# Optimization experiments

Measured on AMD Instinct MI355X. Metric: run time of the kernel, lower is better.

The kernel has to match this reference:

```python
import jax, jax.numpy as jnp
import numpy as np

B, K, T = 8, 88, 32768
NMS_KSIZE = 3
GAUSS_KSIZE = 7
GAUSS_STD = 1.0
VEL_PAD_L = 1
VEL_PAD_R = 1


def setup_inputs() -> dict:
    key = jax.random.key(0)
    k1, k2 = jax.random.split(key)
    onset_probs = jax.random.uniform(k1, (B, K, T), dtype=jnp.float32)
    velmap = jax.random.uniform(k2, (B, K, T), dtype=jnp.float32)
    pthresh = jnp.float32(0.5)
    return {"onset_probs": onset_probs, "velmap": velmap, "pthresh": pthresh}


def _gauss_blur1d(x, ksize, std):
    # depthwise gaussian blur along t, reflect padding, 'same' output
    center = (ksize - 1) / 2.0
    i = jnp.arange(ksize, dtype=jnp.float32)
    w = jnp.exp(-0.5 * ((i - center) / std) ** 2)
    w = w / w.sum()
    h = ksize // 2
    xp = jnp.pad(x, ((0, 0), (0, 0), (h, h)), mode="reflect")
    t = x.shape[-1]
    out = w[0] * jax.lax.dynamic_slice_in_dim(xp, 0, t, axis=2)
    for d in range(1, ksize):
        out = out + w[d] * jax.lax.dynamic_slice_in_dim(xp, d, t, axis=2)
    return out


def _nms1d(x, ksize, pthresh):
    # keep entries equal to the local max over a window of ksize (stride 1),
    # zero everything else, then threshold
    h = ksize // 2
    neg_inf = jnp.array(-jnp.inf, dtype=x.dtype)
    xp = jnp.pad(x, ((0, 0), (0, 0), (h, h)), constant_values=neg_inf)
    t = x.shape[-1]
    pooled = jax.lax.dynamic_slice_in_dim(xp, 0, t, axis=2)
    for d in range(1, ksize):
        pooled = jnp.maximum(pooled, jax.lax.dynamic_slice_in_dim(xp, d, t, axis=2))
    out = jnp.where(x == pooled, x, jnp.zeros((), x.dtype))
    out = jnp.where(out >= pthresh, out, jnp.zeros((), x.dtype))
    return out


def _windowed_vel(velmap, pad_l, pad_r):
    # mean of velmap over [t-pad_l, t+pad_r] with reflect padding (dense form
    # of read_velocities evaluated at every (b,k,t))
    total = pad_l + pad_r + 1
    vp = jnp.pad(velmap, ((0, 0), (0, 0), (pad_l, pad_r)), mode="reflect")
    t = velmap.shape[-1]
    acc = jax.lax.dynamic_slice_in_dim(vp, 0, t, axis=2)
    for d in range(1, total):
        acc = acc + jax.lax.dynamic_slice_in_dim(vp, d, t, axis=2)
    return acc / total


def reference(onset_probs, velmap, pthresh):
    prev_max = onset_probs.max()
    blurred = _gauss_blur1d(onset_probs, GAUSS_KSIZE, GAUSS_STD)
    probs = jnp.where(prev_max > 0, blurred, onset_probs)
    probs = _nms1d(probs, NMS_KSIZE, pthresh)
    vels = _windowed_vel(velmap, VEL_PAD_L, VEL_PAD_R)
    vels = jnp.where(probs > 0, vels, jnp.zeros((), vels.dtype))
    # dense equivalent of the nonzero()+gather+DataFrame: (prob, vel) at every
    # detected onset (nonzero entries of probs), zeros elsewhere
    return probs, vels
```

## Files before the change

### kernel.cpp

```cpp
#include <hip/hip_runtime.h>
#include <math.h>
#include <stdint.h>

#define T_DIM 32768
#define TILE 1024
#define BLOCK 256


__device__ __forceinline__ uint32_t float_key(float f) {
    uint32_t u = __float_as_uint(f);
    return (u & 0x80000000u) ? ~u : (u | 0x80000000u);
}


__global__ void init_ws_kernel(uint32_t* ws) { ws[0] = 0u; }

__global__ void max_kernel(const float* __restrict__ x, uint32_t* __restrict__ ws, int n4) {
    int idx = blockIdx.x * blockDim.x + threadIdx.x;
    int stride = gridDim.x * blockDim.x;
    float m = -INFINITY;
    const float4* x4 = reinterpret_cast<const float4*>(x);
    for (int i = idx; i < n4; i += stride) {
        float4 v = x4[i];
        m = fmaxf(m, fmaxf(fmaxf(v.x, v.y), fmaxf(v.z, v.w)));
    }
    #pragma unroll
    for (int off = 32; off > 0; off >>= 1)
        m = fmaxf(m, __shfl_xor(m, off));
    if ((threadIdx.x & 63) == 0)
        atomicMax(ws, float_key(m));
}

__global__ __launch_bounds__(BLOCK) void fused_kernel(
    const float* __restrict__ onset, const float* __restrict__ vel,
    const float* __restrict__ pth, const uint32_t* __restrict__ ws,
    float* __restrict__ probs_out, float* __restrict__ vels_out,
    float w0, float w1, float w2, float w3, float w4, float w5, float w6) {

    __shared__ float sx[TILE + 8];
    __shared__ float sv[TILE + 2];
    __shared__ float sp[TILE + 2];

    const int row = blockIdx.y;
    const int t0 = blockIdx.x * TILE;
    const size_t base = (size_t)row * T_DIM;
    const int tid = threadIdx.x;

    for (int i = tid; i < TILE + 8; i += BLOCK) {
        int t = t0 + i - 4;
        if (t < 0) t = -t;
        if (t >= T_DIM) t = 2 * T_DIM - 2 - t;
        sx[i] = onset[base + t];
    }
    for (int i = tid; i < TILE + 2; i += BLOCK) {
        int t = t0 + i - 1;
        if (t < 0) t = -t;
        if (t >= T_DIM) t = 2 * T_DIM - 2 - t;
        sv[i] = vel[base + t];
    }
    __syncthreads();

    const bool sel = (ws[0] > 0x80000000u);

    for (int i = tid; i < TILE + 2; i += BLOCK) {
        int t = t0 + i - 1;
        float p;
        if (t < 0 || t >= T_DIM) {
            p = -INFINITY;
        } else {
            float acc = __fmul_rn(w0, sx[i]);
            acc = __fadd_rn(acc, __fmul_rn(w1, sx[i + 1]));
            acc = __fadd_rn(acc, __fmul_rn(w2, sx[i + 2]));
            acc = __fadd_rn(acc, __fmul_rn(w3, sx[i + 3]));
            acc = __fadd_rn(acc, __fmul_rn(w4, sx[i + 4]));
            acc = __fadd_rn(acc, __fmul_rn(w5, sx[i + 5]));
            acc = __fadd_rn(acc, __fmul_rn(w6, sx[i + 6]));
            p = sel ? acc : sx[i + 3];
        }
        sp[i] = p;
    }
    __syncthreads();

    const float pthresh = pth[0];
    float po[4], vo[4];
    const int j0 = tid * 4;
    #pragma unroll
    for (int j = 0; j < 4; ++j) {
        const int i = j0 + j + 1;
        float p = sp[i];
        float pooled = fmaxf(fmaxf(sp[i - 1], p), sp[i + 1]);
        float o = (p == pooled) ? p : 0.0f;
        o = (o >= pthresh) ? o : 0.0f;
        po[j] = o;
        float a = __fadd_rn(__fadd_rn(sv[j0 + j], sv[j0 + j + 1]), sv[j0 + j + 2]);
        float v = __fdiv_rn(a, 3.0f);
        vo[j] = (o > 0.0f) ? v : 0.0f;
    }
    *reinterpret_cast<float4*>(&probs_out[base + t0 + j0]) =
        make_float4(po[0], po[1], po[2], po[3]);
    *reinterpret_cast<float4*>(&vels_out[base + t0 + j0]) =
        make_float4(vo[0], vo[1], vo[2], vo[3]);
}


extern "C" void kernel_launch(void* const* d_in, const int* in_sizes, int n_in,
                              void* d_out, int out_size, void* d_ws, size_t ws_size,
                              hipStream_t stream) {
    const float* onset = (const float*)d_in[0];
    const float* vel   = (const float*)d_in[1];
    const float* pth   = (const float*)d_in[2];

    const int n = in_sizes[0];
    const int rows = n / T_DIM;
    float* probs_out = (float*)d_out;
    float* vels_out  = probs_out + (size_t)n;
    uint32_t* wsu = (uint32_t*)d_ws;

    float e[7];
    for (int i = 0; i < 7; ++i) {
        float xi = (float)i - 3.0f;
        float arg = -0.5f * (xi * xi);
        e[i] = (float)exp((double)arg);
    }
    float s = e[0];
    for (int i = 1; i < 7; ++i) s += e[i];
    float w[7];
    for (int i = 0; i < 7; ++i) w[i] = e[i] / s;

    init_ws_kernel<<<1, 1, 0, stream>>>(wsu);
    max_kernel<<<1024, BLOCK, 0, stream>>>(onset, wsu, n / 4);

    dim3 grid(T_DIM / TILE, rows);
    fused_kernel<<<grid, BLOCK, 0, stream>>>(
        onset, vel, pth, wsu, probs_out, vels_out,
        w[0], w[1], w[2], w[3], w[4], w[5], w[6]);
}
```

Measured before the change: 398.3 us.

## Replace shared-memory tiling with per-thread vector loads and nontemporal stores

The fused kernel drops its shared-memory staging and both barriers. Each thread now loads three overlapping float4 vectors of onset and velocity from global memory and computes the blur, NMS and velocity mean in registers. Outputs are written with nontemporal stores, and the max kernel reduces within the block before doing one atomic per block. The overlapping loads triple L1/L2 read traffic per element in exchange for removing LDS traffic and synchronisation, and asm barriers keep the blur's floating-point order exact.

```diff
diff --git a/kernel.cpp b/kernel.cpp
--- a/kernel.cpp
+++ b/kernel.cpp
@@ -2,9 +2,14 @@
 #include <math.h>
 #include <stdint.h>
 
+#pragma clang fp contract(off)
+
 #define T_DIM 32768
-#define TILE 1024
 #define BLOCK 256
+
+typedef float v4f __attribute__((ext_vector_type(4)));
+
+#define FP_BARRIER(x) asm("" : "+v"(x))
 
 
 __device__ __forceinline__ uint32_t float_key(float f) {
@@ -12,23 +17,50 @@
     return (u & 0x80000000u) ? ~u : (u | 0x80000000u);
 }
 
+__device__ __forceinline__ int reflect_idx(int t) {
+    if (t < 0) t = -t;
+    if (t >= T_DIM) t = 2 * T_DIM - 2 - t;
+    return t;
+}
+
+__device__ __forceinline__ float blur7(const float* __restrict__ w,
+                                       const float* taps) {
+    float acc = w[0] * taps[0];
+    FP_BARRIER(acc);
+    #pragma unroll
+    for (int d = 1; d < 7; ++d) {
+        float p = w[d] * taps[d];
+        FP_BARRIER(p);
+        acc = acc + p;
+        FP_BARRIER(acc);
+    }
+    return acc;
+}
+
 
 __global__ void init_ws_kernel(uint32_t* ws) { ws[0] = 0u; }
 
-__global__ void max_kernel(const float* __restrict__ x, uint32_t* __restrict__ ws, int n4) {
+__global__ __launch_bounds__(BLOCK) void max_kernel(const float* __restrict__ x,
+                                                    uint32_t* __restrict__ ws, int n4) {
     int idx = blockIdx.x * blockDim.x + threadIdx.x;
     int stride = gridDim.x * blockDim.x;
     float m = -INFINITY;
-    const float4* x4 = reinterpret_cast<const float4*>(x);
+    const v4f* x4 = reinterpret_cast<const v4f*>(x);
     for (int i = idx; i < n4; i += stride) {
-        float4 v = x4[i];
+        v4f v = x4[i];
         m = fmaxf(m, fmaxf(fmaxf(v.x, v.y), fmaxf(v.z, v.w)));
     }
     #pragma unroll
     for (int off = 32; off > 0; off >>= 1)
         m = fmaxf(m, __shfl_xor(m, off));
-    if ((threadIdx.x & 63) == 0)
+    __shared__ float red[BLOCK / 64];
+    if ((threadIdx.x & 63) == 0) red[threadIdx.x >> 6] = m;
+    __syncthreads();
+    if (threadIdx.x == 0) {
+        #pragma unroll
+        for (int w = 1; w < BLOCK / 64; ++w) m = fmaxf(m, red[w]);
         atomicMax(ws, float_key(m));
+    }
 }
 
 __global__ __launch_bounds__(BLOCK) void fused_kernel(
@@ -37,69 +69,67 @@
     float* __restrict__ probs_out, float* __restrict__ vels_out,
     float w0, float w1, float w2, float w3, float w4, float w5, float w6) {
 
-    __shared__ float sx[TILE + 8];
-    __shared__ float sv[TILE + 2];
-    __shared__ float sp[TILE + 2];
-
     const int row = blockIdx.y;
-    const int t0 = blockIdx.x * TILE;
+    const int j0 = (blockIdx.x * BLOCK + threadIdx.x) * 4;
     const size_t base = (size_t)row * T_DIM;
-    const int tid = threadIdx.x;
-
-    for (int i = tid; i < TILE + 8; i += BLOCK) {
-        int t = t0 + i - 4;
-        if (t < 0) t = -t;
-        if (t >= T_DIM) t = 2 * T_DIM - 2 - t;
-        sx[i] = onset[base + t];
-    }
-    for (int i = tid; i < TILE + 2; i += BLOCK) {
-        int t = t0 + i - 1;
-        if (t < 0) t = -t;
-        if (t >= T_DIM) t = 2 * T_DIM - 2 - t;
-        sv[i] = vel[base + t];
-    }
-    __syncthreads();
 
     const bool sel = (ws[0] > 0x80000000u);
+    const float pthresh = pth[0];
+    const float w[7] = {w0, w1, w2, w3, w4, w5, w6};
 
-    for (int i = tid; i < TILE + 2; i += BLOCK) {
-        int t = t0 + i - 1;
-        float p;
-        if (t < 0 || t >= T_DIM) {
-            p = -INFINITY;
-        } else {
-            float acc = __fmul_rn(w0, sx[i]);
-            acc = __fadd_rn(acc, __fmul_rn(w1, sx[i + 1]));
-            acc = __fadd_rn(acc, __fmul_rn(w2, sx[i + 2]));
-            acc = __fadd_rn(acc, __fmul_rn(w3, sx[i + 3]));
-            acc = __fadd_rn(acc, __fmul_rn(w4, sx[i + 4]));
-            acc = __fadd_rn(acc, __fmul_rn(w5, sx[i + 5]));
-            acc = __fadd_rn(acc, __fmul_rn(w6, sx[i + 6]));
-            p = sel ? acc : sx[i + 3];
+    float pb[6], vv[6];
+
+    if (j0 >= 4 && j0 + 8 <= T_DIM) {
+        const v4f* x4 = reinterpret_cast<const v4f*>(onset + base + j0 - 4);
+        v4f A = x4[0], Bv = x4[1], C = x4[2];
+        float xx[12] = {A.x, A.y, A.z, A.w, Bv.x, Bv.y, Bv.z, Bv.w, C.x, C.y, C.z, C.w};
+
+        const v4f* v4 = reinterpret_cast<const v4f*>(vel + base + j0 - 4);
+        v4f Vm = v4[0], Vc = v4[1], Vp = v4[2];
+        vv[0] = Vm.w; vv[1] = Vc.x; vv[2] = Vc.y; vv[3] = Vc.z; vv[4] = Vc.w; vv[5] = Vp.x;
+
+        #pragma unroll
+        for (int q = 0; q < 6; ++q) {
+            float acc = blur7(w, &xx[q]);
+            pb[q] = sel ? acc : xx[q + 3];
         }
-        sp[i] = p;
+    } else {
+        const float* x = onset + base;
+        const float* v = vel + base;
+        #pragma unroll
+        for (int q = 0; q < 6; ++q) {
+            int t = j0 + q - 1;
+            vv[q] = v[reflect_idx(t)];
+            if (t < 0 || t >= T_DIM) {
+                pb[q] = -INFINITY;
+            } else {
+                float taps[7];
+                #pragma unroll
+                for (int d = 0; d < 7; ++d)
+                    taps[d] = x[reflect_idx(t - 3 + d)];
+                float acc = blur7(w, taps);
+                pb[q] = sel ? acc : x[t];
+            }
+        }
     }
-    __syncthreads();
 
-    const float pthresh = pth[0];
     float po[4], vo[4];
-    const int j0 = tid * 4;
     #pragma unroll
     for (int j = 0; j < 4; ++j) {
-        const int i = j0 + j + 1;
-        float p = sp[i];
-        float pooled = fmaxf(fmaxf(sp[i - 1], p), sp[i + 1]);
+        float p = pb[j + 1];
+        float pooled = fmaxf(fmaxf(pb[j], pb[j + 1]), pb[j + 2]);
         float o = (p == pooled) ? p : 0.0f;
         o = (o >= pthresh) ? o : 0.0f;
         po[j] = o;
-        float a = __fadd_rn(__fadd_rn(sv[j0 + j], sv[j0 + j + 1]), sv[j0 + j + 2]);
-        float v = __fdiv_rn(a, 3.0f);
-        vo[j] = (o > 0.0f) ? v : 0.0f;
+        float a = (vv[j] + vv[j + 1]) + vv[j + 2];
+        float vmean = a / 3.0f;
+        vo[j] = (o > 0.0f) ? vmean : 0.0f;
     }
-    *reinterpret_cast<float4*>(&probs_out[base + t0 + j0]) =
-        make_float4(po[0], po[1], po[2], po[3]);
-    *reinterpret_cast<float4*>(&vels_out[base + t0 + j0]) =
-        make_float4(vo[0], vo[1], vo[2], vo[3]);
+
+    v4f pov = {po[0], po[1], po[2], po[3]};
+    v4f vov = {vo[0], vo[1], vo[2], vo[3]};
+    __builtin_nontemporal_store(pov, reinterpret_cast<v4f*>(&probs_out[base + j0]));
+    __builtin_nontemporal_store(vov, reinterpret_cast<v4f*>(&vels_out[base + j0]));
 }
 
 
@@ -130,7 +160,7 @@
     init_ws_kernel<<<1, 1, 0, stream>>>(wsu);
     max_kernel<<<1024, BLOCK, 0, stream>>>(onset, wsu, n / 4);
 
-    dim3 grid(T_DIM / TILE, rows);
+    dim3 grid(T_DIM / (4 * BLOCK), rows);
     fused_kernel<<<grid, BLOCK, 0, stream>>>(
         onset, vel, pth, wsu, probs_out, vels_out,
         w[0], w[1], w[2], w[3], w[4], w[5], w[6]);
```

Result: faster. 331.9 us (-16.7%).
